# Kernel optimization log

Hardware: AMD Instinct MI355X
Metric: run time of the kernel (lower is better)

## Reference

```python
import jax, jax.numpy as jnp
import numpy as np

# ---- static frequency grid from init kwargs ----
POS_FREQS = 31
W_MIN, W_MAX = 0.1, 1.0
PATCH = 16

def _build_grid():
    g = (W_MAX / W_MIN) ** (1.0 / (POS_FREQS - 1))
    pos_w = (W_MIN * g ** np.arange(POS_FREQS)).astype(np.float32)
    Wx = np.concatenate([-pos_w[::-1], [0.0], pos_w]).astype(np.float32)  # len 63
    Wy = np.concatenate([[0.0], pos_w]).astype(np.float32)               # len 32
    pad_h = (PATCH - len(Wx) % PATCH) % PATCH  # 1 -> H=64
    pad_w = (PATCH - len(Wy) % PATCH) % PATCH  # 0 -> W=32
    U, V = np.meshgrid(Wx, Wy, indexing='ij')
    U = np.pad(U, ((0, pad_h), (0, pad_w))).astype(np.float32)
    V = np.pad(V, ((0, pad_h), (0, pad_w))).astype(np.float32)
    pad_mask = np.ones_like(U)
    if pad_h > 0:
        pad_mask[-pad_h:, :] = 0.0
    if pad_w > 0:
        pad_mask[:, -pad_w:] = 0.0
    return U, V, pad_mask

_U, _V, _PADMASK = _build_grid()
H, W = _U.shape


def _cft_triangles(tris):
    """Closed-form CFT of each triangle over the HxW frequency grid.
    tris: [T,3,2] float32 -> [T,H,W] complex64."""
    pi = np.float32(np.pi)
    U = jnp.asarray(_U)[None]  # [1,H,W]
    V = jnp.asarray(_V)[None]
    xq = tris[:, 0, 0][:, None, None]; yq = tris[:, 0, 1][:, None, None]
    xr = tris[:, 1, 0][:, None, None]; yr = tris[:, 1, 1][:, None, None]
    xs = tris[:, 2, 0][:, None, None]; ys = tris[:, 2, 1][:, None, None]
    det = xq * (yr - ys) + xr * (ys - yq) + xs * (yq - yr)
    area = jnp.abs(0.5 * det)  # [T,1,1]
    U_ = U * (xr - xq) + V * (yr - yq)  # [T,H,W]
    V_ = U * (xs - xr) + V * (ys - yr)
    phase_shift = jnp.exp(-2j * pi * (U * xq + V * yq))
    zero_mask = (U_ == 0) & (V_ == 0)
    diag_mask = (U_ + V_ == 0) & ~zero_mask
    u_mask = (U_ == 0) & ~zero_mask
    v_mask = (V_ == 0) & ~zero_mask
    normal_mask = ~(diag_mask | zero_mask | u_mask | v_mask)
    four_pi2 = np.float32(4.0) * pi * pi

    def inv_safe(den, m):
        # masked reciprocal with safe denominator (keeps grads finite)
        return jnp.where(m, 1.0, 0.0) / jnp.where(m, den, 1.0)

    part1 = (inv_safe(four_pi2 * U_ * V_ * (U_ + V_), normal_mask)
             - inv_safe(four_pi2 * U_ * U_, diag_mask)
             - inv_safe(four_pi2 * V_ * V_, u_mask)
             + inv_safe(four_pi2 * U_ * U_, v_mask))
    base_u = jnp.exp(-2j * pi * U_)
    base_v = jnp.exp(-2j * pi * V_)
    base_uv = jnp.exp(-2j * pi * (U_ + V_))
    j2pi = 2j * pi
    part2 = (jnp.where(normal_mask, -U_ * base_uv + (U_ + V_) * base_u - V_, 0.0)
             + jnp.where(diag_mask, base_u + j2pi * U_ - 1.0, 0.0)
             + jnp.where(u_mask, base_v + j2pi * V_ - 1.0, 0.0)
             + jnp.where(v_mask, (j2pi * U_ + 1.0) * base_u - 1.0, 0.0))
    FT = 2.0 * area * part1 * part2 * phase_shift
    FT = jnp.where(zero_mask, area.astype(jnp.complex64), FT)
    return FT * jnp.asarray(_PADMASK)[None]


def _forward(batch_triangles, lengths):
    B, maxN = batch_triangles.shape[:2]
    FT = _cft_triangles(batch_triangles.reshape(B * maxN, 3, 2))
    FT = FT.reshape(B, maxN, H, W)
    valid = (jnp.arange(maxN)[None, :] < lengths[:, None]).astype(jnp.float32)
    FT_total = jnp.sum(FT * valid[:, :, None, None], axis=1)  # segment-sum by polygon
    re, im = FT_total.real, FT_total.imag
    m2 = re * re + im * im
    is0 = m2 == 0
    mag = jnp.where(is0, 0.0, jnp.sqrt(jnp.where(is0, 1.0, m2)))
    phase = jnp.arctan2(im, jnp.where(is0, 1.0, re))  # angle(0)=0 like torch
    mag = jnp.log1p(mag)
    return mag[:, None], phase[:, None]  # [B,1,H,W] each


def setup_inputs() -> dict:
    key = jax.random.key(0)
    k1, k2 = jax.random.split(key)
    batch_triangles = jax.random.normal(k1, (64, 128, 3, 2), dtype=jnp.float32)
    lengths = jax.random.randint(k2, (64,), 0, 128, dtype=jnp.int32)
    return {"batch_triangles": batch_triangles, "lengths": lengths}


def reference(batch_triangles, lengths):
    return _forward(batch_triangles, lengths)
```

## Files before the change

### kernel.cpp

```cpp
#include <hip/hip_runtime.h>
#include <cmath>

#define BB     64
#define MAXN   128
#define HH     64
#define WW     32
#define NFREQ  (HH*WW)
#define BLK    256
#define PCHUNKS (NFREQ/BLK)
#define TRI_CHUNK 32
#define QQ     (MAXN/TRI_CHUNK)

__device__ __forceinline__ void sincos_2pi(float x, float* s, float* c) {
    float r = __builtin_amdgcn_fractf(x);
    *s = __builtin_amdgcn_sinf(r);
    *c = __builtin_amdgcn_cosf(r);
}

__global__ __launch_bounds__(BLK) void poly_cft_partial(
    const float* __restrict__ tris,
    const int*   __restrict__ lengths,
    float2*      __restrict__ ws)
{
    __shared__ float4 sA[TRI_CHUNK];
    __shared__ float4 sB[TRI_CHUNK];
    __shared__ float  s_posw[31];

    const int pc = blockIdx.x;
    const int q  = blockIdx.y;
    const int b  = blockIdx.z;
    const int p  = (pc << 8) | threadIdx.x;
    const int h  = p >> 5;
    const int w  = p & 31;

    const int N   = lengths[b];
    const int n0  = q * TRI_CHUNK;
    const int cnt = min(n0 + TRI_CHUNK, N) - n0;

    if (threadIdx.x < 31) {
        double g = pow(10.0, 1.0 / 30.0);
        s_posw[threadIdx.x] = (float)(0.1 * pow(g, (double)threadIdx.x));
    }

    if ((int)threadIdx.x < cnt) {
        const float* t = tris + ((size_t)b * MAXN + n0 + threadIdx.x) * 6;
        float xq = t[0], yq = t[1];
        float xr = t[2], yr = t[3];
        float xs = t[4], ys = t[5];
        float det  = xq * (yr - ys) + xr * (ys - yq) + xs * (yq - yr);
        float area = fabsf(0.5f * det);
        sA[threadIdx.x] = make_float4(xq, yq, xr - xq, yr - yq);
        sB[threadIdx.x] = make_float4(xs - xr, ys - yr, area, 0.0f);
    }
    __syncthreads();

    float U;
    if (h < 31)       U = -s_posw[30 - h];
    else if (h == 31) U = 0.0f;
    else if (h < 63)  U = s_posw[h - 32];
    else              U = 0.0f;
    const float V = (w == 0) ? 0.0f : s_posw[w - 1];

    const float PI_F     = 3.14159274101257324f;
    const float TWOPI    = 6.28318548202514648f;
    const float FOUR_PI2 = (4.0f * PI_F) * PI_F;

    float accR = 0.0f, accI = 0.0f;

    for (int n = 0; n < cnt; ++n) {
        const float4 A  = sA[n];
        const float4 Bv = sB[n];
        const float xq = A.x,  yq = A.y,  e1x = A.z, e1y = A.w;
        const float e2x = Bv.x, e2y = Bv.y, area = Bv.z;

        const float U_ = __fadd_rn(__fmul_rn(U, e1x), __fmul_rn(V, e1y));
        const float V_ = __fadd_rn(__fmul_rn(U, e2x), __fmul_rn(V, e2y));
        const float S  = __fadd_rn(U_, V_);

        const bool uz = (U_ == 0.0f);
        const bool vz = (V_ == 0.0f);

        if (uz && vz) {
            accR += area;
        } else {
            float su, cu, sv, cv, sp, cp;
            sincos_2pi(U_, &su, &cu);
            sincos_2pi(V_, &sv, &cv);
            const float t = U * xq + V * yq;
            sincos_2pi(t, &sp, &cp);

            float p1, p2r, p2i;
            if (S == 0.0f) {
                p1  = -__builtin_amdgcn_rcpf(FOUR_PI2 * U_ * U_);
                p2r = cu - 1.0f;
                p2i = TWOPI * U_ - su;
            } else if (uz) {
                p1  = -__builtin_amdgcn_rcpf(FOUR_PI2 * V_ * V_);
                p2r = cv - 1.0f;
                p2i = TWOPI * V_ - sv;
            } else if (vz) {
                p1  = __builtin_amdgcn_rcpf(FOUR_PI2 * U_ * U_);
                p2r = cu + TWOPI * U_ * su - 1.0f;
                p2i = TWOPI * U_ * cu - su;
            } else {
                const float cuv = cu * cv - su * sv;
                const float suv = su * cv + cu * sv;
                p1  = __builtin_amdgcn_rcpf(FOUR_PI2 * U_ * V_ * S);
                p2r = -U_ * cuv + S * cu - V_;
                p2i =  U_ * suv - S * su;
            }

            const float k   = 2.0f * area * p1;
            accR += k * (p2r * cp + p2i * sp);
            accI += k * (p2i * cp - p2r * sp);
        }
    }

    ws[((size_t)q * BB + b) * NFREQ + p] = make_float2(accR, accI);
}

__global__ __launch_bounds__(BLK) void poly_cft_finalize(
    const float2* __restrict__ ws,
    float*        __restrict__ out)
{
    const int idx = blockIdx.x * BLK + threadIdx.x;
    const int b = idx >> 11;
    const int p = idx & (NFREQ - 1);
    const int h = p >> 5;

    float accR = 0.0f, accI = 0.0f;
#pragma unroll
    for (int q = 0; q < QQ; ++q) {
        float2 v = ws[((size_t)q * BB + b) * NFREQ + p];
        accR += v.x;
        accI += v.y;
    }

    if (h == 63) { accR = 0.0f; accI = 0.0f; }

    const float m2 = __fadd_rn(__fmul_rn(accR, accR), __fmul_rn(accI, accI));
    float mag, ph;
    if (m2 == 0.0f) {
        mag = 0.0f;
        ph  = atan2f(accI, 1.0f);
    } else {
        mag = log1pf(sqrtf(m2));
        ph  = atan2f(accI, accR);
    }

    out[idx]              = mag;
    out[BB * NFREQ + idx] = ph;
}

extern "C" void kernel_launch(void* const* d_in, const int* in_sizes, int n_in,
                              void* d_out, int out_size, void* d_ws, size_t ws_size,
                              hipStream_t stream) {
    const float* tris    = (const float*)d_in[0];
    const int*   lengths = (const int*)d_in[1];
    float*       out     = (float*)d_out;
    float2*      partial = (float2*)d_ws;

    poly_cft_partial<<<dim3(PCHUNKS, QQ, BB), dim3(BLK), 0, stream>>>(tris, lengths, partial);
    poly_cft_finalize<<<dim3(BB * NFREQ / BLK), dim3(BLK), 0, stream>>>(partial, out);
}
```

Measured before the change: 83.57 us.

## Make triangle evaluation branchless via vertex-phase identity, halve chunk, skip empty chunks

The per-triangle CFT is rewritten as a branchless linear combination of sin/cos at the three vertex phases, using coefficients chosen per mask case. This replaces the divergent if/else chain and the extra complex multiply. The triangle chunk is halved to 16, and the loop is unrolled over a fixed count with zero-padded shared slots. Blocks whose chunk holds no valid triangles now exit early, and the finalize kernel sums only the chunks that were written. These steps cut wasted work on padding and branch divergence, at the cost of more partial writes and slightly different rounding in the phase terms.

```diff
diff --git a/kernel.cpp b/kernel.cpp
--- a/kernel.cpp
+++ b/kernel.cpp
@@ -8,13 +8,64 @@
 #define NFREQ  (HH*WW)
 #define BLK    256
 #define PCHUNKS (NFREQ/BLK)
-#define TRI_CHUNK 32
+#define TRI_CHUNK 16
 #define QQ     (MAXN/TRI_CHUNK)
 
 __device__ __forceinline__ void sincos_2pi(float x, float* s, float* c) {
     float r = __builtin_amdgcn_fractf(x);
     *s = __builtin_amdgcn_sinf(r);
     *c = __builtin_amdgcn_cosf(r);
+}
+
+__device__ __forceinline__ void eval_tri(
+    float U, float V, float4 A4, float4 B4, float& accR, float& accI,
+    float TWOPI, float FOUR_PI2)
+{
+    const float xq = A4.x,  yq = A4.y,  e1x = A4.z, e1y = A4.w;
+    const float e2x = B4.x, e2y = B4.y, area = B4.z;
+
+    const float U_ = __fadd_rn(__fmul_rn(U, e1x), __fmul_rn(V, e1y));
+    const float V_ = __fadd_rn(__fmul_rn(U, e2x), __fmul_rn(V, e2y));
+    const float S  = __fadd_rn(U_, V_);
+
+    const bool uz   = (U_ == 0.0f);
+    const bool vz   = (V_ == 0.0f);
+    const bool sz   = (S  == 0.0f);
+    const bool zero = uz && vz;
+    const bool diag = sz && !zero;
+    const bool u_m  = uz && !zero;
+    const bool v_m  = vz && !zero;
+    const bool nrm  = !(uz || vz || sz);
+
+    const float t_q = U * xq + V * yq;
+    const float t_r = t_q + U_;
+    const float t_s = t_r + V_;
+
+    float s_q, c_q, s_r, c_r, s_s, c_s;
+    sincos_2pi(t_q, &s_q, &c_q);
+    sincos_2pi(t_r, &s_r, &c_r);
+    sincos_2pi(t_s, &s_s, &c_s);
+
+    const float twU = TWOPI * U_;
+    const float twV = TWOPI * V_;
+
+    const float Ac = nrm ? -U_ : (u_m ? 1.0f : 0.0f);
+    const float Bc = nrm ?  S  : ((diag || v_m) ? 1.0f : 0.0f);
+    const float Cc = nrm ? -V_ : -1.0f;
+    const float Dc = v_m  ? twU : 0.0f;
+    const float Ec = diag ? twU : (u_m ? twV : 0.0f);
+
+    const float d1  = u_m ? V_ : U_;
+    const float den = nrm ? (U_ * V_) * S : d1 * d1;
+    const float p1  = __builtin_amdgcn_rcpf(FOUR_PI2 * den);
+    const float sgn = (diag || u_m) ? -2.0f : 2.0f;
+    const float k   = zero ? 0.0f : sgn * area * p1;
+
+    const float re =  Ac * c_s + Bc * c_r + Cc * c_q + Dc * s_r + Ec * s_q;
+    const float im = -(Ac * s_s + Bc * s_r + Cc * s_q) + Dc * c_r + Ec * c_q;
+
+    accR = fmaf(k, re, accR) + (zero ? area : 0.0f);
+    accI = fmaf(k, im, accI);
 }
 
 __global__ __launch_bounds__(BLK) void poly_cft_partial(
@@ -37,20 +88,27 @@
     const int n0  = q * TRI_CHUNK;
     const int cnt = min(n0 + TRI_CHUNK, N) - n0;
 
+    if (cnt <= 0) return;
+
     if (threadIdx.x < 31) {
         double g = pow(10.0, 1.0 / 30.0);
         s_posw[threadIdx.x] = (float)(0.1 * pow(g, (double)threadIdx.x));
     }
 
-    if ((int)threadIdx.x < cnt) {
-        const float* t = tris + ((size_t)b * MAXN + n0 + threadIdx.x) * 6;
-        float xq = t[0], yq = t[1];
-        float xr = t[2], yr = t[3];
-        float xs = t[4], ys = t[5];
-        float det  = xq * (yr - ys) + xr * (ys - yq) + xs * (yq - yr);
-        float area = fabsf(0.5f * det);
-        sA[threadIdx.x] = make_float4(xq, yq, xr - xq, yr - yq);
-        sB[threadIdx.x] = make_float4(xs - xr, ys - yr, area, 0.0f);
+    if (threadIdx.x < TRI_CHUNK) {
+        if ((int)threadIdx.x < cnt) {
+            const float* t = tris + ((size_t)b * MAXN + n0 + threadIdx.x) * 6;
+            float xq = t[0], yq = t[1];
+            float xr = t[2], yr = t[3];
+            float xs = t[4], ys = t[5];
+            float det  = xq * (yr - ys) + xr * (ys - yq) + xs * (yq - yr);
+            float area = fabsf(0.5f * det);
+            sA[threadIdx.x] = make_float4(xq, yq, xr - xq, yr - yq);
+            sB[threadIdx.x] = make_float4(xs - xr, ys - yr, area, 0.0f);
+        } else {
+            sA[threadIdx.x] = make_float4(0.0f, 0.0f, 0.0f, 0.0f);
+            sB[threadIdx.x] = make_float4(0.0f, 0.0f, 0.0f, 0.0f);
+        }
     }
     __syncthreads();
 
@@ -67,53 +125,9 @@
 
     float accR = 0.0f, accI = 0.0f;
 
-    for (int n = 0; n < cnt; ++n) {
-        const float4 A  = sA[n];
-        const float4 Bv = sB[n];
-        const float xq = A.x,  yq = A.y,  e1x = A.z, e1y = A.w;
-        const float e2x = Bv.x, e2y = Bv.y, area = Bv.z;
-
-        const float U_ = __fadd_rn(__fmul_rn(U, e1x), __fmul_rn(V, e1y));
-        const float V_ = __fadd_rn(__fmul_rn(U, e2x), __fmul_rn(V, e2y));
-        const float S  = __fadd_rn(U_, V_);
-
-        const bool uz = (U_ == 0.0f);
-        const bool vz = (V_ == 0.0f);
-
-        if (uz && vz) {
-            accR += area;
-        } else {
-            float su, cu, sv, cv, sp, cp;
-            sincos_2pi(U_, &su, &cu);
-            sincos_2pi(V_, &sv, &cv);
-            const float t = U * xq + V * yq;
-            sincos_2pi(t, &sp, &cp);
-
-            float p1, p2r, p2i;
-            if (S == 0.0f) {
-                p1  = -__builtin_amdgcn_rcpf(FOUR_PI2 * U_ * U_);
-                p2r = cu - 1.0f;
-                p2i = TWOPI * U_ - su;
-            } else if (uz) {
-                p1  = -__builtin_amdgcn_rcpf(FOUR_PI2 * V_ * V_);
-                p2r = cv - 1.0f;
-                p2i = TWOPI * V_ - sv;
-            } else if (vz) {
-                p1  = __builtin_amdgcn_rcpf(FOUR_PI2 * U_ * U_);
-                p2r = cu + TWOPI * U_ * su - 1.0f;
-                p2i = TWOPI * U_ * cu - su;
-            } else {
-                const float cuv = cu * cv - su * sv;
-                const float suv = su * cv + cu * sv;
-                p1  = __builtin_amdgcn_rcpf(FOUR_PI2 * U_ * V_ * S);
-                p2r = -U_ * cuv + S * cu - V_;
-                p2i =  U_ * suv - S * su;
-            }
-
-            const float k   = 2.0f * area * p1;
-            accR += k * (p2r * cp + p2i * sp);
-            accI += k * (p2i * cp - p2r * sp);
-        }
+#pragma unroll 4
+    for (int n = 0; n < TRI_CHUNK; ++n) {
+        eval_tri(U, V, sA[n], sB[n], accR, accI, TWOPI, FOUR_PI2);
     }
 
     ws[((size_t)q * BB + b) * NFREQ + p] = make_float2(accR, accI);
@@ -121,6 +135,7 @@
 
 __global__ __launch_bounds__(BLK) void poly_cft_finalize(
     const float2* __restrict__ ws,
+    const int*    __restrict__ lengths,
     float*        __restrict__ out)
 {
     const int idx = blockIdx.x * BLK + threadIdx.x;
@@ -128,9 +143,10 @@
     const int p = idx & (NFREQ - 1);
     const int h = p >> 5;
 
+    const int QN = (lengths[b] + TRI_CHUNK - 1) / TRI_CHUNK;
+
     float accR = 0.0f, accI = 0.0f;
-#pragma unroll
-    for (int q = 0; q < QQ; ++q) {
+    for (int q = 0; q < QN; ++q) {
         float2 v = ws[((size_t)q * BB + b) * NFREQ + p];
         accR += v.x;
         accI += v.y;
@@ -161,5 +177,5 @@
     float2*      partial = (float2*)d_ws;
 
     poly_cft_partial<<<dim3(PCHUNKS, QQ, BB), dim3(BLK), 0, stream>>>(tris, lengths, partial);
-    poly_cft_finalize<<<dim3(BB * NFREQ / BLK), dim3(BLK), 0, stream>>>(partial, out);
+    poly_cft_finalize<<<dim3(BB * NFREQ / BLK), dim3(BLK), 0, stream>>>(partial, lengths, out);
 }
```

New measurement: 79.17 us. 5.3% less time.
